# Optimization experiments

Measured on AMD Instinct MI355X. Metric: run time of the kernel, lower is better.

## Reference

```python
import jax, jax.numpy as jnp
import numpy as np

N_NODES = 100000   # num_nodes
N_EDGES = 50000    # num_hyperedges
M = 1600000        # num incidences
D = 64             # hidden_size
N_LAYERS = 1


def setup_inputs() -> dict:
    key = jax.random.key(0)
    k1, k2, k3 = jax.random.split(key, 3)
    x = jax.random.normal(k1, (N_NODES, D), dtype=jnp.float32)
    node_idx = jax.random.randint(k2, (M,), 0, N_NODES, dtype=jnp.int32)
    edge_idx = jax.random.randint(k3, (M,), 0, N_EDGES, dtype=jnp.int32)
    edge_weight = jnp.ones((N_EDGES,), dtype=jnp.float32)
    return {"x": x, "node_idx": node_idx, "edge_idx": edge_idx, "edge_weight": edge_weight}


def _safe_recip(v):
    # 1/v with inf -> 0, matching D[D==inf]=0
    return jnp.where(v > 0, 1.0 / jnp.where(v > 0, v, 1.0), 0.0)


def _hconv(x, node_idx, edge_idx, edge_weight):
    # D[n] = sum over incidences (n,e) of w[e]; B[e] = hyperedge cardinality
    Dn = jax.ops.segment_sum(edge_weight[edge_idx], node_idx, num_segments=N_NODES)
    Dn = _safe_recip(Dn)
    Be = jax.ops.segment_sum(jnp.ones((node_idx.shape[0],), x.dtype), edge_idx, num_segments=N_EDGES)
    Be = _safe_recip(Be)
    # stage 1: nodes -> hyperedges, message = B[e] * x[j]
    edge_feat = jax.ops.segment_sum(x[node_idx] * Be[edge_idx][:, None], edge_idx, num_segments=N_EDGES)
    # stage 2: hyperedges -> nodes, message = D[i] * edge_feat[e]
    out = jax.ops.segment_sum(edge_feat[edge_idx] * Dn[node_idx][:, None], node_idx, num_segments=N_NODES)
    return out


def reference(x, node_idx, edge_idx, edge_weight):
    h = x
    acc = x
    for _ in range(N_LAYERS):
        h = _hconv(h, node_idx, edge_idx, edge_weight)
        acc = acc + h
    return acc / (N_LAYERS + 1)
```

## Files before the change

### kernel.cpp

```cpp
#include <hip/hip_runtime.h>

#define N_NODES 100000
#define N_EDGES 50000
#define N_KEYS  150000
#define M_INC   1600000
#define D_HID   64

#define SUBR    32
#define SUBLEN  50000
#define KPART   65536
#define PN      2
#define PE      1

#define N_TILES_N 25
#define N_TILES_E 13

typedef float v2f __attribute__((ext_vector_type(2)));


__device__ __forceinline__ unsigned enc_fp8x4(float a, float b, float c, float d) {
    unsigned r = 0;
    r = __builtin_amdgcn_cvt_pk_fp8_f32(a, b, r, false);
    r = __builtin_amdgcn_cvt_pk_fp8_f32(c, d, r, true);
    return r;
}

__global__ __launch_bounds__(1024) void count_kernel(
        const int* __restrict__ node_idx, const int* __restrict__ edge_idx,
        unsigned char* __restrict__ rank_n, unsigned char* __restrict__ rank_e,
        unsigned short* __restrict__ cnt_g) {
    __shared__ unsigned int h[KPART / 4];
    int bid = blockIdx.x;
    const int* idx; unsigned char* rk; int p, s, klim, goff;
    if (bid < PN * SUBR) {
        p = bid / SUBR; s = bid % SUBR;
        idx = node_idx; rk = rank_n; klim = N_NODES; goff = 0;
    } else {
        int b2 = bid - PN * SUBR;
        p = b2 / SUBR; s = b2 % SUBR;
        idx = edge_idx; rk = rank_e; klim = N_EDGES; goff = N_NODES;
    }
    int kbase = p * KPART;
    int t = threadIdx.x;
    for (int i = t; i < KPART / 4; i += 1024) h[i] = 0;
    __syncthreads();
    int mbase = s * SUBLEN;
    const int4* src4 = (const int4*)(idx + mbase);
    for (int i = t; i < SUBLEN / 4; i += 1024) {
        int4 v = src4[i];
        int m0 = mbase + i * 4;
        int k;
        k = v.x - kbase;
        if ((unsigned)k < KPART) {
            unsigned sh = 8u * (k & 3);
            unsigned old = atomicAdd(&h[k >> 2], 1u << sh);
            rk[m0 + 0] = (unsigned char)(old >> sh);
        }
        k = v.y - kbase;
        if ((unsigned)k < KPART) {
            unsigned sh = 8u * (k & 3);
            unsigned old = atomicAdd(&h[k >> 2], 1u << sh);
            rk[m0 + 1] = (unsigned char)(old >> sh);
        }
        k = v.z - kbase;
        if ((unsigned)k < KPART) {
            unsigned sh = 8u * (k & 3);
            unsigned old = atomicAdd(&h[k >> 2], 1u << sh);
            rk[m0 + 2] = (unsigned char)(old >> sh);
        }
        k = v.w - kbase;
        if ((unsigned)k < KPART) {
            unsigned sh = 8u * (k & 3);
            unsigned old = atomicAdd(&h[k >> 2], 1u << sh);
            rk[m0 + 3] = (unsigned char)(old >> sh);
        }
    }
    __syncthreads();
    for (int i = t; i < KPART; i += 1024) {
        int key = kbase + i;
        if (key < klim)
            cnt_g[s * N_KEYS + goff + key] =
                (unsigned short)((h[i >> 2] >> (8u * (i & 3))) & 0xFFu);
    }
}

__global__ void replprefix_kernel(const unsigned short* __restrict__ cnt_g,
                                  unsigned short* __restrict__ rb, int* __restrict__ tot) {
    int key = blockIdx.x * 256 + threadIdx.x;
    if (key < N_KEYS) {
        int base = 0;
#pragma unroll
        for (int k = 0; k < SUBR; k++) {
            rb[k * N_KEYS + key] = (unsigned short)base;
            base += (int)cnt_g[k * N_KEYS + key];
        }
        tot[key] = base;
    }
}

__global__ void scan_partial_kernel(const int* __restrict__ cnt,
                                    int* __restrict__ pn, int* __restrict__ pe) {
    __shared__ int lds[16];
    int b = blockIdx.x;
    const int* src; int nElem; int tile; int* dst;
    if (b < N_TILES_N) { src = cnt;            nElem = N_NODES; tile = b;             dst = pn; }
    else               { src = cnt + N_NODES;  nElem = N_EDGES; tile = b - N_TILES_N; dst = pe; }
    int t = threadIdx.x;
    int i4 = tile * 1024 + t;
    int sum = 0;
    if (i4 * 4 < nElem) {
        int4 v = ((const int4*)src)[i4];
        sum = v.x + v.y + v.z + v.w;
    }
    for (int off = 1; off < 64; off <<= 1) sum += __shfl_xor(sum, off, 64);
    if ((t & 63) == 0) lds[t >> 6] = sum;
    __syncthreads();
    if (t < 16) {
        int s = lds[t];
        for (int off = 1; off < 16; off <<= 1) s += __shfl_xor(s, off, 64);
        if (t == 0) dst[tile] = s;
    }
}

__global__ void scan_base_kernel(const int* __restrict__ pn, const int* __restrict__ pe,
                                 int* __restrict__ bn, int* __restrict__ be,
                                 int* __restrict__ noff, int* __restrict__ eoff) {
    int w = threadIdx.x >> 6;
    int lane = threadIdx.x & 63;
    if (w == 0) {
        int v = (lane < N_TILES_N) ? pn[lane] : 0;
        int incl = v;
        for (int d = 1; d < 64; d <<= 1) { int u = __shfl_up(incl, d, 64); if (lane >= d) incl += u; }
        if (lane < N_TILES_N) bn[lane] = incl - v;
        if (lane == N_TILES_N - 1) noff[N_NODES] = incl;
    } else {
        int v = (lane < N_TILES_E) ? pe[lane] : 0;
        int incl = v;
        for (int d = 1; d < 64; d <<= 1) { int u = __shfl_up(incl, d, 64); if (lane >= d) incl += u; }
        if (lane < N_TILES_E) be[lane] = incl - v;
        if (lane == N_TILES_E - 1) eoff[N_EDGES] = incl;
    }
}

__global__ void scan_write_kernel(const int* __restrict__ cnt,
                                  const int* __restrict__ bn, const int* __restrict__ be,
                                  int* __restrict__ noff, int* __restrict__ eoff) {
    __shared__ int wsum[16];
    int b = blockIdx.x;
    const int* src; int* dst; int nElem; int tile; int tbase;
    if (b < N_TILES_N) { src = cnt;           dst = noff; nElem = N_NODES; tile = b;             tbase = bn[tile]; }
    else               { src = cnt + N_NODES; dst = eoff; nElem = N_EDGES; tile = b - N_TILES_N; tbase = be[tile]; }
    int t = threadIdx.x;
    int lane = t & 63, w = t >> 6;
    int i4 = tile * 1024 + t;
    int4 c = make_int4(0, 0, 0, 0);
    bool valid = (i4 * 4 < nElem);
    if (valid) c = ((const int4*)src)[i4];
    int tsum = c.x + c.y + c.z + c.w;
    int incl = tsum;
    for (int d = 1; d < 64; d <<= 1) { int u = __shfl_up(incl, d, 64); if (lane >= d) incl += u; }
    if (lane == 63) wsum[w] = incl;
    __syncthreads();
    if (t < 16) {
        int v = wsum[t];
        int wi = v;
        for (int d = 1; d < 16; d <<= 1) { int u = __shfl_up(wi, d, 64); if (t >= d) wi += u; }
        wsum[t] = wi - v;
    }
    __syncthreads();
    int ex = tbase + wsum[w] + incl - tsum;
    if (valid) {
        int4 o;
        o.x = ex; o.y = ex + c.x; o.z = o.y + c.y; o.w = o.z + c.z;
        ((int4*)dst)[i4] = o;
    }
}

__global__ void fill_kernel(const int* __restrict__ node_idx,
                            const int* __restrict__ edge_idx,
                            const unsigned char* __restrict__ rank_n,
                            const unsigned char* __restrict__ rank_e,
                            const unsigned short* __restrict__ rb,
                            const int* __restrict__ noff, const int* __restrict__ eoff,
                            int* __restrict__ node_csr, int* __restrict__ edge_csr) {
    int q = blockIdx.x * 256 + threadIdx.x;
    if (q < M_INC / 4) {
        int m0 = q * 4;
        int s = m0 / SUBLEN;
        const unsigned short* rbs = rb + s * N_KEYS;
        int4 nv = ((const int4*)node_idx)[q];
        int4 ev = ((const int4*)edge_idx)[q];
        uchar4 rn = ((const uchar4*)rank_n)[q];
        uchar4 re = ((const uchar4*)rank_e)[q];
        node_csr[noff[nv.x] + (int)rbs[nv.x] + (int)rn.x] = ev.x;
        node_csr[noff[nv.y] + (int)rbs[nv.y] + (int)rn.y] = ev.y;
        node_csr[noff[nv.z] + (int)rbs[nv.z] + (int)rn.z] = ev.z;
        node_csr[noff[nv.w] + (int)rbs[nv.w] + (int)rn.w] = ev.w;
        edge_csr[eoff[ev.x] + (int)rbs[N_NODES + ev.x] + (int)re.x] = nv.x;
        edge_csr[eoff[ev.y] + (int)rbs[N_NODES + ev.y] + (int)re.y] = nv.y;
        edge_csr[eoff[ev.z] + (int)rbs[N_NODES + ev.z] + (int)re.z] = nv.z;
        edge_csr[eoff[ev.w] + (int)rbs[N_NODES + ev.w] + (int)re.w] = nv.w;
    }
}

__global__ void cvt_kernel(const float* __restrict__ x, uint2* __restrict__ xh) {
    int i = blockIdx.x * 256 + threadIdx.x;
    if (i < (N_NODES * D_HID) / 8) {
        const float4* x4 = (const float4*)x;
        float4 a = x4[i * 2], b = x4[i * 2 + 1];
        uint2 o;
        o.x = enc_fp8x4(a.x, a.y, a.z, a.w);
        o.y = enc_fp8x4(b.x, b.y, b.z, b.w);
        xh[i] = o;
    }
}

__global__ void stage1_kernel(const int* __restrict__ eoff, const int* __restrict__ ecsr,
                              const uint2* __restrict__ xh, uint2* __restrict__ ef) {
    int wid = (blockIdx.x * 256 + threadIdx.x) >> 6;
    if (wid >= N_EDGES) return;
    int lane = threadIdx.x & 63;
    int group = lane >> 3;
    int gl = lane & 7;
    int s = eoff[wid], t = eoff[wid + 1];
    float acc[8] = {0.f, 0.f, 0.f, 0.f, 0.f, 0.f, 0.f, 0.f};
    for (int base = s; base < t; base += 64) {
        int idx_l = (base + lane < t) ? ecsr[base + lane] : 0;
        int cnt = t - base; if (cnt > 64) cnt = 64;
        int steps = (cnt + 7) >> 3;
        for (int j = 0; j < steps; j++) {
            int p = 8 * j + group;
            int mi = __shfl(idx_l, p, 64);
            if (p < cnt) {
                uint2 v = xh[(size_t)mi * 8 + gl];
                v2f d0 = __builtin_amdgcn_cvt_pk_f32_fp8(v.x, false);
                v2f d1 = __builtin_amdgcn_cvt_pk_f32_fp8(v.x, true);
                v2f d2 = __builtin_amdgcn_cvt_pk_f32_fp8(v.y, false);
                v2f d3 = __builtin_amdgcn_cvt_pk_f32_fp8(v.y, true);
                acc[0] += d0.x; acc[1] += d0.y; acc[2] += d1.x; acc[3] += d1.y;
                acc[4] += d2.x; acc[5] += d2.y; acc[6] += d3.x; acc[7] += d3.y;
            }
        }
    }
    for (int off = 8; off < 64; off <<= 1)
#pragma unroll
        for (int i = 0; i < 8; i++) acc[i] += __shfl_xor(acc[i], off, 64);
    if (group == 0) {
        int card = t - s;
        float ber = (card > 0) ? (1.0f / (float)card) : 0.f;
        uint2 o;
        o.x = enc_fp8x4(acc[0] * ber, acc[1] * ber, acc[2] * ber, acc[3] * ber);
        o.y = enc_fp8x4(acc[4] * ber, acc[5] * ber, acc[6] * ber, acc[7] * ber);
        ef[(size_t)wid * 8 + gl] = o;
    }
}

__global__ void stage2_kernel(const int* __restrict__ noff, const int* __restrict__ ncsr,
                              const uint2* __restrict__ ef, const float* __restrict__ ew,
                              const float* __restrict__ x, float* __restrict__ out) {
    int wid = (blockIdx.x * 256 + threadIdx.x) >> 6;
    if (wid >= N_NODES) return;
    int lane = threadIdx.x & 63;
    int group = lane >> 3;
    int gl = lane & 7;
    int s = noff[wid], t = noff[wid + 1];
    float acc[8] = {0.f, 0.f, 0.f, 0.f, 0.f, 0.f, 0.f, 0.f};
    float dn = 0.f;
    for (int base = s; base < t; base += 64) {
        bool lv = (base + lane < t);
        int idx_l = lv ? ncsr[base + lane] : 0;
        if (lv) dn += ew[idx_l];
        int cnt = t - base; if (cnt > 64) cnt = 64;
        int steps = (cnt + 7) >> 3;
        for (int j = 0; j < steps; j++) {
            int p = 8 * j + group;
            int mi = __shfl(idx_l, p, 64);
            if (p < cnt) {
                uint2 v = ef[(size_t)mi * 8 + gl];
                v2f d0 = __builtin_amdgcn_cvt_pk_f32_fp8(v.x, false);
                v2f d1 = __builtin_amdgcn_cvt_pk_f32_fp8(v.x, true);
                v2f d2 = __builtin_amdgcn_cvt_pk_f32_fp8(v.y, false);
                v2f d3 = __builtin_amdgcn_cvt_pk_f32_fp8(v.y, true);
                acc[0] += d0.x; acc[1] += d0.y; acc[2] += d1.x; acc[3] += d1.y;
                acc[4] += d2.x; acc[5] += d2.y; acc[6] += d3.x; acc[7] += d3.y;
            }
        }
    }
    for (int off = 1; off < 64; off <<= 1) dn += __shfl_xor(dn, off, 64);
    for (int off = 8; off < 64; off <<= 1)
#pragma unroll
        for (int i = 0; i < 8; i++) acc[i] += __shfl_xor(acc[i], off, 64);
    if (group == 0) {
        float dnr = (dn > 0.f) ? (1.0f / dn) : 0.f;
        const float4* x4 = (const float4*)x;
        float4* o4 = (float4*)out;
        float4 a = x4[(size_t)wid * 16 + gl * 2];
        float4 b = x4[(size_t)wid * 16 + gl * 2 + 1];
        float4 ra, rb2;
        ra.x = 0.5f * (a.x + dnr * acc[0]);
        ra.y = 0.5f * (a.y + dnr * acc[1]);
        ra.z = 0.5f * (a.z + dnr * acc[2]);
        ra.w = 0.5f * (a.w + dnr * acc[3]);
        rb2.x = 0.5f * (b.x + dnr * acc[4]);
        rb2.y = 0.5f * (b.y + dnr * acc[5]);
        rb2.z = 0.5f * (b.z + dnr * acc[6]);
        rb2.w = 0.5f * (b.w + dnr * acc[7]);
        o4[(size_t)wid * 16 + gl * 2] = ra;
        o4[(size_t)wid * 16 + gl * 2 + 1] = rb2;
    }
}

extern "C" void kernel_launch(void* const* d_in, const int* in_sizes, int n_in,
                              void* d_out, int out_size, void* d_ws, size_t ws_size,
                              hipStream_t stream) {
    const float* x        = (const float*)d_in[0];
    const int*   node_idx = (const int*)d_in[1];
    const int*   edge_idx = (const int*)d_in[2];
    const float* ew       = (const float*)d_in[3];
    float* out = (float*)d_out;

    char* ws = (char*)d_ws;
    unsigned char*  rank_n   = (unsigned char*)(ws + 0);
    unsigned char*  rank_e   = (unsigned char*)(ws + 1600000);
    int*            noff     = (int*)(ws + 3200000);
    int*            eoff     = (int*)(ws + 3600016);
    int*            node_csr = (int*)(ws + 3800032);
    int*            edge_csr = (int*)(ws + 10200032);
    unsigned short* cnt_g = (unsigned short*)(ws + 3800032);
    unsigned short* rb    = (unsigned short*)(ws + 16600032);
    int*            pn    = (int*)(ws + 26200032);
    int*            pe    = pn + 32;
    int*            bn    = pn + 64;
    int*            be    = pn + 96;
    int*            tot   = (int*)(ws + 26204128);
    uint2*          ef    = (uint2*)(ws + 0);
    uint2*          xh    = (uint2*)(ws + 16600032);

    count_kernel<<<(PN + PE) * SUBR, 1024, 0, stream>>>(node_idx, edge_idx, rank_n, rank_e, cnt_g);
    replprefix_kernel<<<(N_KEYS + 255) / 256, 256, 0, stream>>>(cnt_g, rb, tot);
    scan_partial_kernel<<<N_TILES_N + N_TILES_E, 1024, 0, stream>>>(tot, pn, pe);
    scan_base_kernel<<<1, 128, 0, stream>>>(pn, pe, bn, be, noff, eoff);
    scan_write_kernel<<<N_TILES_N + N_TILES_E, 1024, 0, stream>>>(tot, bn, be, noff, eoff);
    fill_kernel<<<(M_INC / 4 + 255) / 256, 256, 0, stream>>>(node_idx, edge_idx, rank_n, rank_e,
                                                             rb, noff, eoff, node_csr, edge_csr);
    cvt_kernel<<<((N_NODES * D_HID / 8) + 255) / 256, 256, 0, stream>>>(x, xh);
    stage1_kernel<<<(N_EDGES * 64 + 255) / 256, 256, 0, stream>>>(eoff, edge_csr, xh, ef);
    stage2_kernel<<<(N_NODES * 64 + 255) / 256, 256, 0, stream>>>(noff, node_csr, ef, ew, x, out);
}
```

Measured before the change: 258.3 us.

## Replace random CSR fill with two-pass bucketed scatter and 16-bit node CSR

Replaces the single fill kernel, which scatters 3.2M ints to random CSR slots, with a two-pass binning scheme. The first pass groups packed (local slot, value) words into 128 output buckets per CSR using LDS histograms and global atomic cursors. The second pass scatters each bucket into a 50KB-local region, so the writes stay cache-friendly. Node CSR entries are also narrowed to 16-bit, since edge ids are below 65536, which cuts stage2 index traffic. The cost is an extra kernel pass, an extra write and read of the intermediate bins, and more atomics.

```diff
diff --git a/kernel.cpp b/kernel.cpp
--- a/kernel.cpp
+++ b/kernel.cpp
@@ -14,6 +14,9 @@
 
 #define N_TILES_N 25
 #define N_TILES_E 13
+
+#define NBKT    128
+#define BKT_SZ  12500
 
 typedef float v2f __attribute__((ext_vector_type(2)));
 
@@ -124,21 +127,26 @@
 
 __global__ void scan_base_kernel(const int* __restrict__ pn, const int* __restrict__ pe,
                                  int* __restrict__ bn, int* __restrict__ be,
-                                 int* __restrict__ noff, int* __restrict__ eoff) {
-    int w = threadIdx.x >> 6;
-    int lane = threadIdx.x & 63;
-    if (w == 0) {
+                                 int* __restrict__ noff, int* __restrict__ eoff,
+                                 int* __restrict__ cur) {
+    int t = threadIdx.x;
+    int lane = t & 63;
+    if (t < 64) {
         int v = (lane < N_TILES_N) ? pn[lane] : 0;
         int incl = v;
         for (int d = 1; d < 64; d <<= 1) { int u = __shfl_up(incl, d, 64); if (lane >= d) incl += u; }
         if (lane < N_TILES_N) bn[lane] = incl - v;
         if (lane == N_TILES_N - 1) noff[N_NODES] = incl;
-    } else {
+    } else if (t < 128) {
         int v = (lane < N_TILES_E) ? pe[lane] : 0;
         int incl = v;
         for (int d = 1; d < 64; d <<= 1) { int u = __shfl_up(incl, d, 64); if (lane >= d) incl += u; }
         if (lane < N_TILES_E) be[lane] = incl - v;
         if (lane == N_TILES_E - 1) eoff[N_EDGES] = incl;
+    } else {
+        int i = t - 128;
+        cur[i] = i * BKT_SZ;
+        cur[i + NBKT] = i * BKT_SZ;
     }
 }
 
@@ -176,30 +184,90 @@
     }
 }
 
-__global__ void fill_kernel(const int* __restrict__ node_idx,
-                            const int* __restrict__ edge_idx,
-                            const unsigned char* __restrict__ rank_n,
-                            const unsigned char* __restrict__ rank_e,
-                            const unsigned short* __restrict__ rb,
-                            const int* __restrict__ noff, const int* __restrict__ eoff,
-                            int* __restrict__ node_csr, int* __restrict__ edge_csr) {
-    int q = blockIdx.x * 256 + threadIdx.x;
-    if (q < M_INC / 4) {
-        int m0 = q * 4;
-        int s = m0 / SUBLEN;
-        const unsigned short* rbs = rb + s * N_KEYS;
-        int4 nv = ((const int4*)node_idx)[q];
-        int4 ev = ((const int4*)edge_idx)[q];
-        uchar4 rn = ((const uchar4*)rank_n)[q];
-        uchar4 re = ((const uchar4*)rank_e)[q];
-        node_csr[noff[nv.x] + (int)rbs[nv.x] + (int)rn.x] = ev.x;
-        node_csr[noff[nv.y] + (int)rbs[nv.y] + (int)rn.y] = ev.y;
-        node_csr[noff[nv.z] + (int)rbs[nv.z] + (int)rn.z] = ev.z;
-        node_csr[noff[nv.w] + (int)rbs[nv.w] + (int)rn.w] = ev.w;
-        edge_csr[eoff[ev.x] + (int)rbs[N_NODES + ev.x] + (int)re.x] = nv.x;
-        edge_csr[eoff[ev.y] + (int)rbs[N_NODES + ev.y] + (int)re.y] = nv.y;
-        edge_csr[eoff[ev.z] + (int)rbs[N_NODES + ev.z] + (int)re.z] = nv.z;
-        edge_csr[eoff[ev.w] + (int)rbs[N_NODES + ev.w] + (int)re.w] = nv.w;
+__global__ __launch_bounds__(512) void binA_kernel(
+        const int* __restrict__ node_idx, const int* __restrict__ edge_idx,
+        const unsigned char* __restrict__ rank_n, const unsigned char* __restrict__ rank_e,
+        const unsigned short* __restrict__ rb,
+        const int* __restrict__ noff, const int* __restrict__ eoff,
+        int* __restrict__ cur,
+        unsigned int* __restrict__ bin_n, unsigned int* __restrict__ bin_e) {
+    __shared__ unsigned int hist[2 * NBKT];
+    __shared__ unsigned int gbase[2 * NBKT];
+    int t = threadIdx.x;
+    if (t < 2 * NBKT) hist[t] = 0;
+    __syncthreads();
+    unsigned pk[16];
+    unsigned mt[16];
+    int cbase = blockIdx.x * 1024;
+#pragma unroll
+    for (int j = 0; j < 2; j++) {
+        int q = cbase + t * 2 + j;
+        bool valid = q < M_INC / 4;
+        int4 nv = make_int4(0, 0, 0, 0), ev = make_int4(0, 0, 0, 0);
+        uchar4 rn = make_uchar4(0, 0, 0, 0), re = make_uchar4(0, 0, 0, 0);
+        const unsigned short* rbs = rb;
+        if (valid) {
+            nv = ((const int4*)node_idx)[q];
+            ev = ((const int4*)edge_idx)[q];
+            rn = ((const uchar4*)rank_n)[q];
+            re = ((const uchar4*)rank_e)[q];
+            rbs = rb + ((q * 4) / SUBLEN) * N_KEYS;
+        }
+        int ns[4] = {nv.x, nv.y, nv.z, nv.w};
+        int es[4] = {ev.x, ev.y, ev.z, ev.w};
+        int rns[4] = {rn.x, rn.y, rn.z, rn.w};
+        int res[4] = {re.x, re.y, re.z, re.w};
+#pragma unroll
+        for (int k = 0; k < 4; k++) {
+            int idxn = j * 8 + k, idxe = j * 8 + 4 + k;
+            if (valid) {
+                int n = ns[k], e = es[k];
+                int slot = noff[n] + (int)rbs[n] + rns[k];
+                int b = slot / BKT_SZ;
+                unsigned lr = atomicAdd(&hist[b], 1u);
+                pk[idxn] = ((unsigned)(slot - b * BKT_SZ) << 17) | (unsigned)e;
+                mt[idxn] = ((unsigned)b << 13) | lr;
+                slot = eoff[e] + (int)rbs[N_NODES + e] + res[k];
+                b = slot / BKT_SZ;
+                lr = atomicAdd(&hist[NBKT + b], 1u);
+                pk[idxe] = ((unsigned)(slot - b * BKT_SZ) << 17) | (unsigned)n;
+                mt[idxe] = ((unsigned)(NBKT + b) << 13) | lr;
+            } else {
+                mt[idxn] = 0xFFFFFFFFu;
+                mt[idxe] = 0xFFFFFFFFu;
+            }
+        }
+    }
+    __syncthreads();
+    if (t < 2 * NBKT) gbase[t] = (unsigned)atomicAdd(&cur[t], (int)hist[t]);
+    __syncthreads();
+#pragma unroll
+    for (int i = 0; i < 16; i++) {
+        if (mt[i] != 0xFFFFFFFFu) {
+            unsigned b = mt[i] >> 13;
+            unsigned pos = gbase[b] + (mt[i] & 0x1FFFu);
+            if (b < NBKT) bin_n[pos] = pk[i];
+            else          bin_e[pos] = pk[i];
+        }
+    }
+}
+
+__global__ __launch_bounds__(512) void binB_kernel(
+        const unsigned int* __restrict__ bin_n, const unsigned int* __restrict__ bin_e,
+        unsigned short* __restrict__ node_csr, int* __restrict__ edge_csr) {
+    int b = blockIdx.x;
+    if (b < NBKT) {
+        int base = b * BKT_SZ;
+        for (int i = threadIdx.x; i < BKT_SZ; i += 512) {
+            unsigned p = bin_n[base + i];
+            node_csr[base + (int)(p >> 17)] = (unsigned short)(p & 0x1FFFFu);
+        }
+    } else {
+        int base = (b - NBKT) * BKT_SZ;
+        for (int i = threadIdx.x; i < BKT_SZ; i += 512) {
+            unsigned p = bin_e[base + i];
+            edge_csr[base + (int)(p >> 17)] = (int)(p & 0x1FFFFu);
+        }
     }
 }
 
@@ -255,7 +323,7 @@
     }
 }
 
-__global__ void stage2_kernel(const int* __restrict__ noff, const int* __restrict__ ncsr,
+__global__ void stage2_kernel(const int* __restrict__ noff, const unsigned short* __restrict__ ncsr,
                               const uint2* __restrict__ ef, const float* __restrict__ ew,
                               const float* __restrict__ x, float* __restrict__ out) {
     int wid = (blockIdx.x * 256 + threadIdx.x) >> 6;
@@ -268,7 +336,7 @@
     float dn = 0.f;
     for (int base = s; base < t; base += 64) {
         bool lv = (base + lane < t);
-        int idx_l = lv ? ncsr[base + lane] : 0;
+        int idx_l = lv ? (int)ncsr[base + lane] : 0;
         if (lv) dn += ew[idx_l];
         int cnt = t - base; if (cnt > 64) cnt = 64;
         int steps = (cnt + 7) >> 3;
@@ -324,25 +392,29 @@
     unsigned char*  rank_e   = (unsigned char*)(ws + 1600000);
     int*            noff     = (int*)(ws + 3200000);
     int*            eoff     = (int*)(ws + 3600016);
-    int*            node_csr = (int*)(ws + 3800032);
-    int*            edge_csr = (int*)(ws + 10200032);
-    unsigned short* cnt_g = (unsigned short*)(ws + 3800032);
-    unsigned short* rb    = (unsigned short*)(ws + 16600032);
-    int*            pn    = (int*)(ws + 26200032);
-    int*            pe    = pn + 32;
-    int*            bn    = pn + 64;
-    int*            be    = pn + 96;
-    int*            tot   = (int*)(ws + 26204128);
+    int*            cur      = (int*)(ws + 3800032);
+    int*            pn       = (int*)(ws + 3801056);
+    int*            pe       = pn + 32;
+    int*            bn       = pn + 64;
+    int*            be       = pn + 96;
+    unsigned short* node_csr = (unsigned short*)(ws + 3801600);
+    int*            edge_csr = (int*)(ws + 7001600);
+    unsigned short* rb       = (unsigned short*)(ws + 13401600);
+    unsigned int*   bin_n    = (unsigned int*)(ws + 23001600);
+    unsigned int*   bin_e    = (unsigned int*)(ws + 29401600);
+    unsigned short* cnt_g = (unsigned short*)(ws + 23001600);
+    int*            tot   = (int*)(ws + 3801600);
     uint2*          ef    = (uint2*)(ws + 0);
-    uint2*          xh    = (uint2*)(ws + 16600032);
+    uint2*          xh    = (uint2*)(ws + 13401600);
 
     count_kernel<<<(PN + PE) * SUBR, 1024, 0, stream>>>(node_idx, edge_idx, rank_n, rank_e, cnt_g);
     replprefix_kernel<<<(N_KEYS + 255) / 256, 256, 0, stream>>>(cnt_g, rb, tot);
     scan_partial_kernel<<<N_TILES_N + N_TILES_E, 1024, 0, stream>>>(tot, pn, pe);
-    scan_base_kernel<<<1, 128, 0, stream>>>(pn, pe, bn, be, noff, eoff);
+    scan_base_kernel<<<1, 256, 0, stream>>>(pn, pe, bn, be, noff, eoff, cur);
     scan_write_kernel<<<N_TILES_N + N_TILES_E, 1024, 0, stream>>>(tot, bn, be, noff, eoff);
-    fill_kernel<<<(M_INC / 4 + 255) / 256, 256, 0, stream>>>(node_idx, edge_idx, rank_n, rank_e,
-                                                             rb, noff, eoff, node_csr, edge_csr);
+    binA_kernel<<<(M_INC / 4 + 1023) / 1024, 512, 0, stream>>>(node_idx, edge_idx, rank_n, rank_e,
+                                                               rb, noff, eoff, cur, bin_n, bin_e);
+    binB_kernel<<<2 * NBKT, 512, 0, stream>>>(bin_n, bin_e, node_csr, edge_csr);
     cvt_kernel<<<((N_NODES * D_HID / 8) + 255) / 256, 256, 0, stream>>>(x, xh);
     stage1_kernel<<<(N_EDGES * 64 + 255) / 256, 256, 0, stream>>>(eoff, edge_csr, xh, ef);
     stage2_kernel<<<(N_NODES * 64 + 255) / 256, 256, 0, stream>>>(noff, node_csr, ef, ew, x, out);
```

Result: slower. 266.6 us (+3.2%).
